# Performance work log

Measured on AMD Instinct MI355X. Metric: run time of the kernel, lower is better.

## Reference

```python
import jax, jax.numpy as jnp
import numpy as np

DARK_VALUE = 1.0
K = 20  # max_patch_size


def setup_inputs() -> dict:
    key = jax.random.key(0)
    x = jax.random.uniform(key, (32, 3, 512, 512), dtype=jnp.float32)
    return {"x": x}


def reference(x):
    pl = (K - 1) // 2  # 9  (torch pads left/top by (k-1)//2)
    pr = K // 2        # 10 (right/bottom by k//2)
    # replicate pad on H, W
    xp = jnp.pad(x, ((0, 0), (0, 0), (pl, pr), (pl, pr)), mode='edge')
    # erosion: -maxpool(-x) == sliding min over KxK window, stride 1, VALID
    eroded = jax.lax.reduce_window(
        xp, jnp.array(jnp.inf, xp.dtype), jax.lax.min,
        window_dimensions=(1, 1, K, K), window_strides=(1, 1, 1, 1),
        padding='VALID')  # [B, C, H, W]
    dark = jnp.min(eroded, axis=1)  # channel-min -> [B, H, W]
    return jnp.abs(DARK_VALUE - jnp.mean(dark))
```

## Files before the change

### kernel.cpp

```cpp
#include <hip/hip_runtime.h>
#include <hip/hip_fp16.h>
#include <math.h>


#define BATCH 32
#define HH 512
#define WW 512
#define CH (HH * WW)

__device__ __forceinline__ float fmin3(float a, float b, float c) {
    return fminf(fminf(a, b), c);
}

__device__ __forceinline__ unsigned pkmin(unsigned a, unsigned b) {
    unsigned r;
    asm volatile("v_pk_min_f16 %0, %1, %2" : "=v"(r) : "v"(a), "v"(b));
    return r;
}

__device__ __forceinline__ float2 unpack_h2(unsigned u) {
    __half2 h;
    *(unsigned*)&h = u;
    return __half22float2(h);
}

__launch_bounds__(256)
__global__ void hmin_kernel(const float* __restrict__ x, __half* __restrict__ hm)
{
    int gid = blockIdx.x * 256 + threadIdx.x;
    int r = gid & 31;
    int h = (gid >> 5) & (HH - 1);
    int b = gid >> 14;
    int j0 = r << 4;

    const float* row = x + (size_t)b * 3 * CH + (size_t)h * WW;

    int cb  = j0 - 12;
    int cbc = cb < 0 ? 0 : (cb > WW - 40 ? WW - 40 : cb);
    const float4* p0 = (const float4*)(row + cbc);
    const float4* p1 = (const float4*)(row + cbc + CH);
    const float4* p2 = (const float4*)(row + cbc + 2 * CH);
    float e[40];
    #pragma unroll
    for (int k = 0; k < 10; ++k) {
        float4 a = p0[k], bb = p1[k], c = p2[k];
        e[4 * k + 0] = fmin3(a.x, bb.x, c.x);
        e[4 * k + 1] = fmin3(a.y, bb.y, c.y);
        e[4 * k + 2] = fmin3(a.z, bb.z, c.z);
        e[4 * k + 3] = fmin3(a.w, bb.w, c.w);
    }

    float w[35];
    if (r == 0) {
        #pragma unroll
        for (int d = 0; d < 35; ++d) w[d] = e[d < 9 ? 0 : d - 9];
    } else if (r == 31) {
        #pragma unroll
        for (int d = 0; d < 35; ++d) w[d] = e[d + 15 > 39 ? 39 : d + 15];
    } else {
        #pragma unroll
        for (int d = 0; d < 35; ++d) w[d] = e[d + 3];
    }

    float suf[20];
    suf[19] = w[19];
    #pragma unroll
    for (int k = 18; k >= 0; --k) suf[k] = fminf(w[k], suf[k + 1]);
    float pre[15];
    pre[0] = w[20];
    #pragma unroll
    for (int k = 1; k < 15; ++k) pre[k] = fminf(pre[k - 1], w[20 + k]);
    float o[16];
    o[0] = suf[0];
    #pragma unroll
    for (int i = 1; i < 16; ++i) o[i] = fminf(suf[i], pre[i - 1]);

    __half2 hp[8];
    #pragma unroll
    for (int k = 0; k < 8; ++k)
        hp[k] = __halves2half2(__float2half_rn(o[2 * k]), __float2half_rn(o[2 * k + 1]));
    float4* dst = (float4*)(hm + ((size_t)b * HH + h) * WW + j0);
    dst[0] = *(float4*)&hp[0];
    dst[1] = *(float4*)&hp[4];
}

__launch_bounds__(256)
__global__ void vmin_kernel(const unsigned* __restrict__ hm2,
                            float* __restrict__ partials)
{
    int gid = blockIdx.x * 256 + threadIdx.x;
    int jj = gid & 255;
    int rr = (gid >> 8) & 31;
    int b  = gid >> 13;
    int i0 = rr << 4;

    const unsigned* col = hm2 + (size_t)b * (CH / 2) + jj;

    int rb  = i0 - 9;
    int rbc = rb < 0 ? 0 : (rb > HH - 35 ? HH - 35 : rb);
    unsigned ld[35];
    #pragma unroll
    for (int d = 0; d < 35; ++d) ld[d] = col[(rbc + d) * (WW / 2)];

    unsigned w[35];
    if (rr == 0) {
        #pragma unroll
        for (int d = 0; d < 35; ++d) w[d] = ld[d < 9 ? 0 : d - 9];
    } else if (rr == 31) {
        #pragma unroll
        for (int d = 0; d < 35; ++d) w[d] = ld[d + 10 > 34 ? 34 : d + 10];
    } else {
        #pragma unroll
        for (int d = 0; d < 35; ++d) w[d] = ld[d];
    }

    unsigned suf[20];
    suf[19] = w[19];
    #pragma unroll
    for (int k = 18; k >= 0; --k) suf[k] = pkmin(w[k], suf[k + 1]);
    unsigned pre[15];
    pre[0] = w[20];
    #pragma unroll
    for (int k = 1; k < 15; ++k) pre[k] = pkmin(pre[k - 1], w[20 + k]);

    float sum;
    {
        float2 f = unpack_h2(suf[0]);
        sum = f.x + f.y;
    }
    #pragma unroll
    for (int i = 1; i < 16; ++i) {
        float2 f = unpack_h2(pkmin(suf[i], pre[i - 1]));
        sum += f.x + f.y;
    }

    #pragma unroll
    for (int off = 32; off; off >>= 1) sum += __shfl_down(sum, off);
    __shared__ float red[4];
    if ((threadIdx.x & 63) == 0) red[threadIdx.x >> 6] = sum;
    __syncthreads();
    if (threadIdx.x == 0)
        partials[blockIdx.x] = red[0] + red[1] + red[2] + red[3];
}

__launch_bounds__(256)
__global__ void dark_reduce_kernel(const float* __restrict__ partials, int n,
                                   float* __restrict__ out)
{
    __shared__ float red[4];
    int t = threadIdx.x;
    float s = 0.f;
    for (int i = t; i < n; i += 256) s += partials[i];
    #pragma unroll
    for (int off = 32; off; off >>= 1) s += __shfl_down(s, off);
    if ((t & 63) == 0) red[t >> 6] = s;
    __syncthreads();
    if (t == 0) {
        float total = red[0] + red[1] + red[2] + red[3];
        float mean = total / (float)((long long)BATCH * HH * WW);
        out[0] = fabsf(1.0f - mean);
    }
}

extern "C" void kernel_launch(void* const* d_in, const int* in_sizes, int n_in,
                              void* d_out, int out_size, void* d_ws, size_t ws_size,
                              hipStream_t stream) {
    const float* x = (const float*)d_in[0];
    float* out = (float*)d_out;

    __half* hm = (__half*)d_ws;
    float* partials = (float*)((char*)d_ws + (size_t)BATCH * CH * 2);

    hmin_kernel<<<2048, 256, 0, stream>>>(x, hm);
    vmin_kernel<<<1024, 256, 0, stream>>>((const unsigned*)hm, partials);
    dark_reduce_kernel<<<1, 256, 0, stream>>>(partials, 1024, out);
}
```

Baseline: 36.32 us.

## Fuse horizontal, vertical min and final reduction into one tiled kernel

Replaces the three-kernel pipeline, which goes through a global fp16 intermediate, with one kernel. Each block handles a 64x64 tile: it computes horizontal mins for 83 halo rows into LDS as fp32, then does the vertical min and sum from LDS. The last block, found with an atomic counter and a threadfence, does the final reduction, removing the global intermediate traffic and extra launches. In exchange, halo rows are recomputed, which means about 30% extra input reads and hmin work per tile. It also adds a memset before the launch and about 22KB of LDS per block, which may limit occupancy.

New measurement: 129.9 us. +257.8%, slower.

```diff
diff --git a/kernel.cpp b/kernel.cpp
--- a/kernel.cpp
+++ b/kernel.cpp
@@ -1,5 +1,4 @@
 #include <hip/hip_runtime.h>
-#include <hip/hip_fp16.h>
 #include <math.h>
 
 
@@ -7,158 +6,130 @@
 #define HH 512
 #define WW 512
 #define CH (HH * WW)
+#define NBX 8
+#define NBY 8
+#define NBLK (NBX * NBY * BATCH)
+#define LSTR 66
 
 __device__ __forceinline__ float fmin3(float a, float b, float c) {
     return fminf(fminf(a, b), c);
 }
 
-__device__ __forceinline__ unsigned pkmin(unsigned a, unsigned b) {
-    unsigned r;
-    asm volatile("v_pk_min_f16 %0, %1, %2" : "=v"(r) : "v"(a), "v"(b));
-    return r;
-}
+__launch_bounds__(256)
+__global__ void dark_fused_kernel(const float* __restrict__ x,
+                                  float* __restrict__ partials,
+                                  unsigned* __restrict__ counter,
+                                  float* __restrict__ out)
+{
+    __shared__ float hm[83 * LSTR];
+    __shared__ float red[4];
+    __shared__ int lastflag;
 
-__device__ __forceinline__ float2 unpack_h2(unsigned u) {
-    __half2 h;
-    *(unsigned*)&h = u;
-    return __half22float2(h);
-}
+    const int b  = blockIdx.z;
+    const int h0 = blockIdx.y * 64;
+    const int w0 = blockIdx.x * 64;
+    const int t  = threadIdx.x;
+    const float* xb = x + (size_t)b * 3 * CH;
 
-__launch_bounds__(256)
-__global__ void hmin_kernel(const float* __restrict__ x, __half* __restrict__ hm)
-{
-    int gid = blockIdx.x * 256 + threadIdx.x;
-    int r = gid & 31;
-    int h = (gid >> 5) & (HH - 1);
-    int b = gid >> 14;
-    int j0 = r << 4;
+    for (int task = t; task < 83 * 4; task += 256) {
+        int r = task >> 2;
+        int q = task & 3;
+        int gr = h0 - 9 + r; gr = gr < 0 ? 0 : (gr > HH - 1 ? HH - 1 : gr);
+        int jg0 = w0 + (q << 4);
+        int grun = jg0 >> 4;
+        const float* row = xb + gr * WW;
+        int cb  = jg0 - 12;
+        int cbc = cb < 0 ? 0 : (cb > WW - 40 ? WW - 40 : cb);
+        const float4* p0 = (const float4*)(row + cbc);
+        const float4* p1 = (const float4*)(row + cbc + CH);
+        const float4* p2 = (const float4*)(row + cbc + 2 * CH);
+        float e[40];
+        #pragma unroll
+        for (int k = 0; k < 10; ++k) {
+            float4 a = p0[k], bb = p1[k], c = p2[k];
+            e[4 * k + 0] = fmin3(a.x, bb.x, c.x);
+            e[4 * k + 1] = fmin3(a.y, bb.y, c.y);
+            e[4 * k + 2] = fmin3(a.z, bb.z, c.z);
+            e[4 * k + 3] = fmin3(a.w, bb.w, c.w);
+        }
+        float w[35];
+        if (grun == 0) {
+            #pragma unroll
+            for (int d = 0; d < 35; ++d) w[d] = e[d < 9 ? 0 : d - 9];
+        } else if (grun == 31) {
+            #pragma unroll
+            for (int d = 0; d < 35; ++d) w[d] = e[d + 15 > 39 ? 39 : d + 15];
+        } else {
+            #pragma unroll
+            for (int d = 0; d < 35; ++d) w[d] = e[d + 3];
+        }
+        float suf[20];
+        suf[19] = w[19];
+        #pragma unroll
+        for (int k = 18; k >= 0; --k) suf[k] = fminf(w[k], suf[k + 1]);
+        float pre[15];
+        pre[0] = w[20];
+        #pragma unroll
+        for (int k = 1; k < 15; ++k) pre[k] = fminf(pre[k - 1], w[20 + k]);
+        float o[16];
+        o[0] = suf[0];
+        #pragma unroll
+        for (int i = 1; i < 16; ++i) o[i] = fminf(suf[i], pre[i - 1]);
 
-    const float* row = x + (size_t)b * 3 * CH + (size_t)h * WW;
+        float* dst = &hm[r * LSTR + (q << 4)];
+        #pragma unroll
+        for (int k = 0; k < 8; ++k)
+            *(float2*)(dst + 2 * k) = make_float2(o[2 * k], o[2 * k + 1]);
+    }
+    __syncthreads();
 
-    int cb  = j0 - 12;
-    int cbc = cb < 0 ? 0 : (cb > WW - 40 ? WW - 40 : cb);
-    const float4* p0 = (const float4*)(row + cbc);
-    const float4* p1 = (const float4*)(row + cbc + CH);
-    const float4* p2 = (const float4*)(row + cbc + 2 * CH);
-    float e[40];
-    #pragma unroll
-    for (int k = 0; k < 10; ++k) {
-        float4 a = p0[k], bb = p1[k], c = p2[k];
-        e[4 * k + 0] = fmin3(a.x, bb.x, c.x);
-        e[4 * k + 1] = fmin3(a.y, bb.y, c.y);
-        e[4 * k + 2] = fmin3(a.z, bb.z, c.z);
-        e[4 * k + 3] = fmin3(a.w, bb.w, c.w);
-    }
-
-    float w[35];
-    if (r == 0) {
+    float sum = 0.f;
+    {
+        int j  = t & 63;
+        int i0 = (t >> 6) << 4;
+        float w[35];
         #pragma unroll
-        for (int d = 0; d < 35; ++d) w[d] = e[d < 9 ? 0 : d - 9];
-    } else if (r == 31) {
+        for (int d = 0; d < 35; ++d) w[d] = hm[(i0 + d) * LSTR + j];
+        float suf[20];
+        suf[19] = w[19];
         #pragma unroll
-        for (int d = 0; d < 35; ++d) w[d] = e[d + 15 > 39 ? 39 : d + 15];
-    } else {
+        for (int k = 18; k >= 0; --k) suf[k] = fminf(w[k], suf[k + 1]);
+        float pre[15];
+        pre[0] = w[20];
         #pragma unroll
-        for (int d = 0; d < 35; ++d) w[d] = e[d + 3];
-    }
-
-    float suf[20];
-    suf[19] = w[19];
-    #pragma unroll
-    for (int k = 18; k >= 0; --k) suf[k] = fminf(w[k], suf[k + 1]);
-    float pre[15];
-    pre[0] = w[20];
-    #pragma unroll
-    for (int k = 1; k < 15; ++k) pre[k] = fminf(pre[k - 1], w[20 + k]);
-    float o[16];
-    o[0] = suf[0];
-    #pragma unroll
-    for (int i = 1; i < 16; ++i) o[i] = fminf(suf[i], pre[i - 1]);
-
-    __half2 hp[8];
-    #pragma unroll
-    for (int k = 0; k < 8; ++k)
-        hp[k] = __halves2half2(__float2half_rn(o[2 * k]), __float2half_rn(o[2 * k + 1]));
-    float4* dst = (float4*)(hm + ((size_t)b * HH + h) * WW + j0);
-    dst[0] = *(float4*)&hp[0];
-    dst[1] = *(float4*)&hp[4];
-}
-
-__launch_bounds__(256)
-__global__ void vmin_kernel(const unsigned* __restrict__ hm2,
-                            float* __restrict__ partials)
-{
-    int gid = blockIdx.x * 256 + threadIdx.x;
-    int jj = gid & 255;
-    int rr = (gid >> 8) & 31;
-    int b  = gid >> 13;
-    int i0 = rr << 4;
-
-    const unsigned* col = hm2 + (size_t)b * (CH / 2) + jj;
-
-    int rb  = i0 - 9;
-    int rbc = rb < 0 ? 0 : (rb > HH - 35 ? HH - 35 : rb);
-    unsigned ld[35];
-    #pragma unroll
-    for (int d = 0; d < 35; ++d) ld[d] = col[(rbc + d) * (WW / 2)];
-
-    unsigned w[35];
-    if (rr == 0) {
+        for (int k = 1; k < 15; ++k) pre[k] = fminf(pre[k - 1], w[20 + k]);
+        sum = suf[0];
         #pragma unroll
-        for (int d = 0; d < 35; ++d) w[d] = ld[d < 9 ? 0 : d - 9];
-    } else if (rr == 31) {
-        #pragma unroll
-        for (int d = 0; d < 35; ++d) w[d] = ld[d + 10 > 34 ? 34 : d + 10];
-    } else {
-        #pragma unroll
-        for (int d = 0; d < 35; ++d) w[d] = ld[d];
-    }
-
-    unsigned suf[20];
-    suf[19] = w[19];
-    #pragma unroll
-    for (int k = 18; k >= 0; --k) suf[k] = pkmin(w[k], suf[k + 1]);
-    unsigned pre[15];
-    pre[0] = w[20];
-    #pragma unroll
-    for (int k = 1; k < 15; ++k) pre[k] = pkmin(pre[k - 1], w[20 + k]);
-
-    float sum;
-    {
-        float2 f = unpack_h2(suf[0]);
-        sum = f.x + f.y;
-    }
-    #pragma unroll
-    for (int i = 1; i < 16; ++i) {
-        float2 f = unpack_h2(pkmin(suf[i], pre[i - 1]));
-        sum += f.x + f.y;
+        for (int i = 1; i < 16; ++i) sum += fminf(suf[i], pre[i - 1]);
     }
 
     #pragma unroll
     for (int off = 32; off; off >>= 1) sum += __shfl_down(sum, off);
-    __shared__ float red[4];
-    if ((threadIdx.x & 63) == 0) red[threadIdx.x >> 6] = sum;
-    __syncthreads();
-    if (threadIdx.x == 0)
-        partials[blockIdx.x] = red[0] + red[1] + red[2] + red[3];
-}
-
-__launch_bounds__(256)
-__global__ void dark_reduce_kernel(const float* __restrict__ partials, int n,
-                                   float* __restrict__ out)
-{
-    __shared__ float red[4];
-    int t = threadIdx.x;
-    float s = 0.f;
-    for (int i = t; i < n; i += 256) s += partials[i];
-    #pragma unroll
-    for (int off = 32; off; off >>= 1) s += __shfl_down(s, off);
-    if ((t & 63) == 0) red[t >> 6] = s;
+    if ((t & 63) == 0) red[t >> 6] = sum;
     __syncthreads();
     if (t == 0) {
-        float total = red[0] + red[1] + red[2] + red[3];
-        float mean = total / (float)((long long)BATCH * HH * WW);
-        out[0] = fabsf(1.0f - mean);
+        float ps = red[0] + red[1] + red[2] + red[3];
+        int bid = (blockIdx.z * NBY + blockIdx.y) * NBX + blockIdx.x;
+        partials[bid] = ps;
+        __threadfence();
+        unsigned old = atomicAdd(counter, 1u);
+        lastflag = (old == NBLK - 1);
+    }
+    __syncthreads();
+
+    if (lastflag) {
+        __threadfence();
+        float s = 0.f;
+        for (int i = t; i < NBLK; i += 256) s += partials[i];
+        #pragma unroll
+        for (int off = 32; off; off >>= 1) s += __shfl_down(s, off);
+        if ((t & 63) == 0) red[t >> 6] = s;
+        __syncthreads();
+        if (t == 0) {
+            float total = red[0] + red[1] + red[2] + red[3];
+            float mean = total / (float)((long long)BATCH * CH);
+            out[0] = fabsf(1.0f - mean);
+        }
     }
 }
 
@@ -167,11 +138,10 @@
                               hipStream_t stream) {
     const float* x = (const float*)d_in[0];
     float* out = (float*)d_out;
+    float* partials = (float*)d_ws;
+    unsigned* counter = (unsigned*)((char*)d_ws + NBLK * 4);
 
-    __half* hm = (__half*)d_ws;
-    float* partials = (float*)((char*)d_ws + (size_t)BATCH * CH * 2);
-
-    hmin_kernel<<<2048, 256, 0, stream>>>(x, hm);
-    vmin_kernel<<<1024, 256, 0, stream>>>((const unsigned*)hm, partials);
-    dark_reduce_kernel<<<1, 256, 0, stream>>>(partials, 1024, out);
+    hipMemsetAsync(counter, 0, 4, stream);
+    dim3 grid(NBX, NBY, BATCH);
+    dark_fused_kernel<<<grid, 256, 0, stream>>>(x, partials, counter, out);
 }
```
